# Kernel optimization log

Measured on AMD Instinct MI355X. Metric: run time of the kernel, lower is better.

Reference implementation:

```python
import jax, jax.numpy as jnp
import numpy as np

D_MODEL = 512
N_HEADS = 8
D_K = 64
D_V = 64
SEQ = 2048
BATCH = 4
WINDOW = 256  # mask_lenth
LN_EPS = 1e-5


def setup_inputs() -> dict:
    key = jax.random.key(0)
    ks = jax.random.split(key, 7)
    s = 1.0 / np.sqrt(D_MODEL)
    return {
        "input_Q": jax.random.normal(ks[0], (BATCH, SEQ, D_MODEL), jnp.float32),
        "input_K": jax.random.normal(ks[1], (BATCH, SEQ, D_MODEL), jnp.float32),
        "input_V": jax.random.normal(ks[2], (BATCH, SEQ, D_MODEL), jnp.float32),
        "W_Q": jax.random.normal(ks[3], (D_MODEL, N_HEADS * D_K), jnp.float32) * s,
        "W_K": jax.random.normal(ks[4], (D_MODEL, N_HEADS * D_K), jnp.float32) * s,
        "W_V": jax.random.normal(ks[5], (D_MODEL, N_HEADS * D_V), jnp.float32) * s,
        "W_fc": jax.random.normal(ks[6], (N_HEADS * D_V, D_MODEL), jnp.float32) * s,
    }


def _band_mask(n, w):
    # keep entries with i-(w-1) <= j <= i  (lower band of width w incl. diagonal)
    i = jnp.arange(n)[:, None]
    j = jnp.arange(n)[None, :]
    return (j <= i) & (j >= i - (w - 1))


def reference(input_Q, input_K, input_V, W_Q, W_K, W_V, W_fc):
    B, L, _ = input_Q.shape
    # projections -> [B, H, L, d]
    Q = (input_Q @ W_Q).reshape(B, L, N_HEADS, D_K).transpose(0, 2, 1, 3)
    K = (input_K @ W_K).reshape(B, L, N_HEADS, D_K).transpose(0, 2, 1, 3)
    V = (input_V @ W_V).reshape(B, L, N_HEADS, D_V).transpose(0, 2, 1, 3)

    scores = jnp.einsum("bhqd,bhkd->bhqk", Q, K) / np.sqrt(D_K)
    mask = _band_mask(L, WINDOW)  # [L, L] bool
    scores = jnp.where(mask[None, None], scores, -jnp.inf)
    attn = jax.nn.softmax(scores, axis=-1)
    context = jnp.einsum("bhqk,bhkd->bhqd", attn, V)  # [B,H,L,d_v]
    context = context.transpose(0, 2, 1, 3).reshape(B, L, N_HEADS * D_V)
    out = context @ W_fc + input_Q  # residual
    # LayerNorm (fresh nn.LayerNorm: gamma=1, beta=0)
    mu = jnp.mean(out, axis=-1, keepdims=True)
    var = jnp.var(out, axis=-1, keepdims=True)
    return (out - mu) * jax.lax.rsqrt(var + LN_EPS)
```

## Files before the change

kernel.cpp:

```cpp
#include <hip/hip_runtime.h>
#include <hip/hip_bf16.h>

#define D_MODEL 512
#define NH      8
#define SEQ     2048
#define BATCH   4
#define WINDOW  256
#define ROWS    (BATCH*SEQ)

typedef __attribute__((ext_vector_type(8))) short bf16x8;
typedef __attribute__((ext_vector_type(4))) float f32x4;
typedef __hip_bfloat16 bf16;

__device__ __forceinline__ f32x4 mfma16(bf16x8 a, bf16x8 b, f32x4 c) {
    return __builtin_amdgcn_mfma_f32_16x16x32_bf16(a, b, c, 0, 0, 0);
}

__device__ __forceinline__ void gload16(const void* g, void* l) {
    __builtin_amdgcn_global_load_lds((const __attribute__((address_space(1))) void*)g,
                                     (__attribute__((address_space(3))) void*)l, 16, 0, 0);
}

__device__ __forceinline__ unsigned f2bf_u(float f) {
    bf16 h = __float2bfloat16(f);
    return (unsigned)(*(unsigned short*)&h);
}

__global__ __launch_bounds__(256)
void wconv(const float* __restrict__ W0, const float* __restrict__ W1,
           const float* __restrict__ W2, const float* __restrict__ W3,
           bf16* __restrict__ Wt) {
    const int z = blockIdx.z;
    const float* W = (z == 0) ? W0 : (z == 1) ? W1 : (z == 2) ? W2 : W3;
    bf16* dst = Wt + (size_t)z * D_MODEL * D_MODEL;

    __shared__ float t[64][65];
    const int k0 = blockIdx.x * 64, n0 = blockIdx.y * 64;
    const int tid = threadIdx.x;

    #pragma unroll
    for (int i = 0; i < 16; ++i) {
        const int e = tid + 256 * i, r = e >> 6, c = e & 63;
        t[r][c] = W[(size_t)(k0 + r) * D_MODEL + n0 + c];
    }
    __syncthreads();
    #pragma unroll
    for (int i = 0; i < 16; ++i) {
        const int e = tid + 256 * i, r = e >> 6, c = e & 63;
        dst[(size_t)(n0 + r) * D_MODEL + k0 + c] = __float2bfloat16(t[c][r]);
    }
}

__global__ __launch_bounds__(256)
void proj_mfma(const float* __restrict__ Xq, const float* __restrict__ Xk,
               const float* __restrict__ Xv, const bf16* __restrict__ Wt,
               bf16* __restrict__ Qp, bf16* __restrict__ Kp, bf16* __restrict__ Vp) {
    const int z = blockIdx.z;
    const float* X = (z == 0) ? Xq : (z == 1) ? Xk : Xv;
    const bf16* W = Wt + (size_t)z * D_MODEL * D_MODEL;
    bf16* outp = (z == 0) ? Qp : (z == 1) ? Kp : Vp;

    __shared__ bf16 Asw[128 * 64];
    __shared__ bf16 Bsw[128 * 64];

    const int tid = threadIdx.x;
    const int lane = tid & 63, w = tid >> 6;
    const int wr = w >> 1, wc = w & 1;
    const int row0 = blockIdx.x * 128, col0 = blockIdx.y * 128;
    const int g = lane >> 4, m16 = lane & 15;

    f32x4 acc[4][4] = {};

    for (int step = 0; step < 8; ++step) {
        const int k0 = step * 64;
        __syncthreads();
        #pragma unroll
        for (int i = 0; i < 4; ++i) {
            const int chunk = i * 256 + w * 64 + lane;
            const int n = chunk >> 3, s = chunk & 7;
            gload16(W + (size_t)(col0 + n) * D_MODEL + k0 + ((s ^ (n & 7)) * 8),
                    &Bsw[(size_t)(i * 256 + w * 64) * 8]);
        }
        #pragma unroll
        for (int i = 0; i < 4; ++i) {
            const int chunk = i * 256 + tid;
            const int m = chunk >> 3, s = chunk & 7;
            const float* gp = X + (size_t)(row0 + m) * D_MODEL + k0 + ((s ^ (m & 7)) * 8);
            const float4 f0 = *(const float4*)gp;
            const float4 f1 = *(const float4*)(gp + 4);
            int4 pk;
            pk.x = f2bf_u(f0.x) | (f2bf_u(f0.y) << 16);
            pk.y = f2bf_u(f0.z) | (f2bf_u(f0.w) << 16);
            pk.z = f2bf_u(f1.x) | (f2bf_u(f1.y) << 16);
            pk.w = f2bf_u(f1.z) | (f2bf_u(f1.w) << 16);
            *(int4*)&Asw[m * 64 + s * 8] = pk;
        }
        __syncthreads();

        #pragma unroll
        for (int c = 0; c < 2; ++c) {
            bf16x8 af[4], bfr[4];
            #pragma unroll
            for (int mi = 0; mi < 4; ++mi) {
                const int m = wr * 64 + mi * 16 + m16;
                const int slot = (c * 4 + g) ^ (m & 7);
                af[mi] = *(const bf16x8*)&Asw[m * 64 + slot * 8];
            }
            #pragma unroll
            for (int ni = 0; ni < 4; ++ni) {
                const int n = wc * 64 + ni * 16 + m16;
                const int slot = (c * 4 + g) ^ (n & 7);
                bfr[ni] = *(const bf16x8*)&Bsw[n * 64 + slot * 8];
            }
            #pragma unroll
            for (int mi = 0; mi < 4; ++mi)
                #pragma unroll
                for (int ni = 0; ni < 4; ++ni)
                    acc[mi][ni] = mfma16(af[mi], bfr[ni], acc[mi][ni]);
        }
    }

    if (z < 2) {
        #pragma unroll
        for (int mi = 0; mi < 4; ++mi)
            #pragma unroll
            for (int ni = 0; ni < 4; ++ni) {
                const int c = col0 + wc * 64 + ni * 16 + m16;
                const int h = c >> 6, d = c & 63;
                #pragma unroll
                for (int reg = 0; reg < 4; ++reg) {
                    const int r = row0 + wr * 64 + mi * 16 + g * 4 + reg;
                    const int b = r >> 11, l = r & (SEQ - 1);
                    outp[(((size_t)b * NH + h) * SEQ + l) * 64 + d] =
                        __float2bfloat16(acc[mi][ni][reg]);
                }
            }
    } else {
        #pragma unroll
        for (int mi = 0; mi < 4; ++mi)
            #pragma unroll
            for (int ni = 0; ni < 4; ++ni) {
                const int c = col0 + wc * 64 + ni * 16 + m16;
                const int h = c >> 6, d = c & 63;
                const int r = row0 + wr * 64 + mi * 16 + g * 4;
                const int b = r >> 11, l = r & (SEQ - 1);
                uint2 pv;
                pv.x = f2bf_u(acc[mi][ni][0]) | (f2bf_u(acc[mi][ni][1]) << 16);
                pv.y = f2bf_u(acc[mi][ni][2]) | (f2bf_u(acc[mi][ni][3]) << 16);
                *(uint2*)&outp[(((size_t)b * NH + h) * 64 + d) * SEQ + l] = pv;
            }
    }
}

__global__ __launch_bounds__(256)
void attn_mfma(const bf16* __restrict__ Qp, const bf16* __restrict__ Kp,
               const bf16* __restrict__ Vp, bf16* __restrict__ ctx) {
    __shared__ bf16 Qs[64][72];
    __shared__ bf16 Ks[64][72];
    __shared__ bf16 Vt[64][72];
    __shared__ bf16 Ps[4][16][72];

    const int bh = blockIdx.y, b = bh >> 3, h = bh & 7;
    const int q0 = blockIdx.x * 64;
    const int tid = threadIdx.x;
    const int lane = tid & 63, w = tid >> 6;
    const int g = lane >> 4, m16 = lane & 15;

    const size_t kvbase = (size_t)bh * SEQ * 64;
    const size_t vtbase = (size_t)bh * 64 * SEQ;

    #pragma unroll
    for (int i = 0; i < 2; ++i) {
        const int chunk = i * 256 + tid, r = chunk >> 3, s = chunk & 7;
        *(int4*)&Qs[r][s * 8] = *(const int4*)(Qp + kvbase + (size_t)(q0 + r) * 64 + s * 8);
    }
    __syncthreads();

    bf16x8 qf[2];
    #pragma unroll
    for (int c = 0; c < 2; ++c)
        qf[c] = *(const bf16x8*)&Qs[w * 16 + m16][c * 32 + g * 8];

    f32x4 o[4] = {};
    float rs = 0.f;

    int klo = q0 - (WINDOW - 1); if (klo < 0) klo = 0;
    const int kt0 = klo >> 6, kt1 = q0 >> 6;
    const int qg = q0 + w * 16 + m16;

    for (int kt = kt0; kt <= kt1; ++kt) {
        const int k0 = kt * 64;
        __syncthreads();
        #pragma unroll
        for (int i = 0; i < 2; ++i) {
            const int chunk = i * 256 + tid, r = chunk >> 3, s = chunk & 7;
            *(int4*)&Ks[r][s * 8] = *(const int4*)(Kp + kvbase + (size_t)(k0 + r) * 64 + s * 8);
            *(int4*)&Vt[r][s * 8] = *(const int4*)(Vp + vtbase + (size_t)r * SEQ + k0 + s * 8);
        }
        __syncthreads();

        f32x4 st[4] = {};
        #pragma unroll
        for (int c = 0; c < 2; ++c) {
            bf16x8 kf[4];
            #pragma unroll
            for (int f = 0; f < 4; ++f)
                kf[f] = *(const bf16x8*)&Ks[f * 16 + m16][c * 32 + g * 8];
            #pragma unroll
            for (int f = 0; f < 4; ++f)
                st[f] = mfma16(kf[f], qf[c], st[f]);
        }

        const int masktype = (k0 == q0) ? 1 : ((k0 < q0 - 192) ? 2 : 0);
        #pragma unroll
        for (int f = 0; f < 4; ++f) {
            float p[4];
            #pragma unroll
            for (int reg = 0; reg < 4; ++reg) {
                const int kg = k0 + f * 16 + g * 4 + reg;
                bool valid = (masktype == 0) || (masktype == 1 ? (kg <= qg)
                                                              : (kg >= qg - (WINDOW - 1)));
                p[reg] = valid ? __expf(st[f][reg] * 0.125f) : 0.f;
                rs += p[reg];
            }
            uint2 pkv;
            pkv.x = f2bf_u(p[0]) | (f2bf_u(p[1]) << 16);
            pkv.y = f2bf_u(p[2]) | (f2bf_u(p[3]) << 16);
            *(uint2*)&Ps[w][m16][f * 16 + g * 4] = pkv;
        }

        #pragma unroll
        for (int c = 0; c < 2; ++c) {
            const bf16x8 pf = *(const bf16x8*)&Ps[w][m16][c * 32 + g * 8];
            #pragma unroll
            for (int f2 = 0; f2 < 4; ++f2) {
                const bf16x8 vf = *(const bf16x8*)&Vt[f2 * 16 + m16][c * 32 + g * 8];
                o[f2] = mfma16(pf, vf, o[f2]);
            }
        }
    }

    rs += __shfl_xor(rs, 16, 64);
    rs += __shfl_xor(rs, 32, 64);
    const float inv = 1.0f / rs;
    float invr[4];
    #pragma unroll
    for (int reg = 0; reg < 4; ++reg)
        invr[reg] = __shfl(inv, g * 4 + reg, 64);

    #pragma unroll
    for (int f2 = 0; f2 < 4; ++f2) {
        const int d = f2 * 16 + m16;
        #pragma unroll
        for (int reg = 0; reg < 4; ++reg) {
            const int qrow = w * 16 + g * 4 + reg;
            ctx[((size_t)b * SEQ + q0 + qrow) * D_MODEL + h * 64 + d] =
                __float2bfloat16(o[f2][reg] * invr[reg]);
        }
    }
}

__global__ __launch_bounds__(256)
void fc_mfma(const bf16* __restrict__ ctx, const bf16* __restrict__ Wt,
             const float* __restrict__ resid, float* __restrict__ out) {
    __shared__ bf16 Asw[128 * 64];
    __shared__ bf16 Bsw[128 * 64];

    const int tid = threadIdx.x;
    const int lane = tid & 63, w = tid >> 6;
    const int wr = w >> 1, wc = w & 1;
    const int row0 = blockIdx.x * 128, col0 = blockIdx.y * 128;
    const int g = lane >> 4, m16 = lane & 15;

    f32x4 acc[4][4] = {};

    for (int step = 0; step < 8; ++step) {
        const int k0 = step * 64;
        __syncthreads();
        #pragma unroll
        for (int i = 0; i < 4; ++i) {
            const int chunk = i * 256 + w * 64 + lane;
            const int m = chunk >> 3, s = chunk & 7;
            gload16(ctx + (size_t)(row0 + m) * D_MODEL + k0 + ((s ^ (m & 7)) * 8),
                    &Asw[(size_t)(i * 256 + w * 64) * 8]);
            gload16(Wt + (size_t)(col0 + m) * D_MODEL + k0 + ((s ^ (m & 7)) * 8),
                    &Bsw[(size_t)(i * 256 + w * 64) * 8]);
        }
        __syncthreads();

        #pragma unroll
        for (int c = 0; c < 2; ++c) {
            bf16x8 af[4], bfr[4];
            #pragma unroll
            for (int mi = 0; mi < 4; ++mi) {
                const int m = wr * 64 + mi * 16 + m16;
                const int slot = (c * 4 + g) ^ (m & 7);
                af[mi] = *(const bf16x8*)&Asw[m * 64 + slot * 8];
            }
            #pragma unroll
            for (int ni = 0; ni < 4; ++ni) {
                const int n = wc * 64 + ni * 16 + m16;
                const int slot = (c * 4 + g) ^ (n & 7);
                bfr[ni] = *(const bf16x8*)&Bsw[n * 64 + slot * 8];
            }
            #pragma unroll
            for (int mi = 0; mi < 4; ++mi)
                #pragma unroll
                for (int ni = 0; ni < 4; ++ni)
                    acc[mi][ni] = mfma16(af[mi], bfr[ni], acc[mi][ni]);
        }
    }

    #pragma unroll
    for (int mi = 0; mi < 4; ++mi)
        #pragma unroll
        for (int ni = 0; ni < 4; ++ni) {
            const int c = col0 + wc * 64 + ni * 16 + m16;
            #pragma unroll
            for (int reg = 0; reg < 4; ++reg) {
                const int r = row0 + wr * 64 + mi * 16 + g * 4 + reg;
                out[(size_t)r * D_MODEL + c] = acc[mi][ni][reg] + resid[(size_t)r * D_MODEL + c];
            }
        }
}

__global__ __launch_bounds__(256)
void ln_kernel(float* __restrict__ out) {
    const int row = blockIdx.x;
    float* p = out + (size_t)row * D_MODEL;
    const int tid = threadIdx.x;

    const float x0 = p[tid], x1 = p[tid + 256];
    float s  = x0 + x1;
    float s2 = x0 * x0 + x1 * x1;
    #pragma unroll
    for (int m = 1; m < 64; m <<= 1) {
        s  += __shfl_xor(s,  m, 64);
        s2 += __shfl_xor(s2, m, 64);
    }
    __shared__ float sa[4], sb[4];
    const int w = tid >> 6;
    if ((tid & 63) == 0) { sa[w] = s; sb[w] = s2; }
    __syncthreads();
    s  = sa[0] + sa[1] + sa[2] + sa[3];
    s2 = sb[0] + sb[1] + sb[2] + sb[3];

    const float mean = s * (1.0f / D_MODEL);
    const float var  = s2 * (1.0f / D_MODEL) - mean * mean;
    const float rstd = rsqrtf(var + 1e-5f);

    p[tid]       = (x0 - mean) * rstd;
    p[tid + 256] = (x1 - mean) * rstd;
}

extern "C" void kernel_launch(void* const* d_in, const int* in_sizes, int n_in,
                              void* d_out, int out_size, void* d_ws, size_t ws_size,
                              hipStream_t stream) {
    const float* inQ = (const float*)d_in[0];
    const float* inK = (const float*)d_in[1];
    const float* inV = (const float*)d_in[2];
    const float* WQ  = (const float*)d_in[3];
    const float* WK  = (const float*)d_in[4];
    const float* WV  = (const float*)d_in[5];
    const float* Wfc = (const float*)d_in[6];
    float* out = (float*)d_out;

    bf16* ws = (bf16*)d_ws;
    const size_t WSZ = (size_t)D_MODEL * D_MODEL;
    const size_t NE  = (size_t)BATCH * NH * SEQ * 64;
    bf16* Wt   = ws;
    bf16* Qp   = ws + 4 * WSZ;
    bf16* Kp   = Qp + NE;
    bf16* Vp   = Kp + NE;
    bf16* ctxb = Vp + NE;

    wconv<<<dim3(8, 8, 4), 256, 0, stream>>>(WQ, WK, WV, Wfc, Wt);
    proj_mfma<<<dim3(ROWS / 128, D_MODEL / 128, 3), 256, 0, stream>>>(
        inQ, inK, inV, Wt, Qp, Kp, Vp);
    attn_mfma<<<dim3(SEQ / 64, BATCH * NH), 256, 0, stream>>>(Qp, Kp, Vp, ctxb);
    fc_mfma<<<dim3(ROWS / 128, D_MODEL / 128), 256, 0, stream>>>(
        ctxb, Wt + 3 * WSZ, inQ, out);
    ln_kernel<<<ROWS, 256, 0, stream>>>(out);
}
```

Measured before the change: 170.7 us.

## Double-buffer LDS tiles in projection, attention and FC kernels to overlap loads

Adds ping-pong shared-memory buffers to the projection, attention and output-FC kernels. The next K-slice or KV tile is prefetched while MFMAs run on the current one, which removes one barrier per iteration. Attention now stages K/V/Q through direct global-to-LDS loads with an XOR swizzle instead of padded arrays. Float-to-bf16 packing uses a paired conversion intrinsic, and LayerNorm uses float2 accesses. The cost is doubled LDS use, which may lower occupancy, and more live registers for the prefetched fp32 A tile.

```diff
diff --git a/kernel.cpp b/kernel.cpp
--- a/kernel.cpp
+++ b/kernel.cpp
@@ -24,6 +24,12 @@
 __device__ __forceinline__ unsigned f2bf_u(float f) {
     bf16 h = __float2bfloat16(f);
     return (unsigned)(*(unsigned short*)&h);
+}
+
+__device__ __forceinline__ unsigned pack2(float lo, float hi) {
+    float2 t; t.x = lo; t.y = hi;
+    __hip_bfloat162 h = __float22bfloat162_rn(t);
+    return *(unsigned*)&h;
 }
 
 __global__ __launch_bounds__(256)
@@ -60,8 +66,8 @@
     const bf16* W = Wt + (size_t)z * D_MODEL * D_MODEL;
     bf16* outp = (z == 0) ? Qp : (z == 1) ? Kp : Vp;
 
-    __shared__ bf16 Asw[128 * 64];
-    __shared__ bf16 Bsw[128 * 64];
+    __shared__ bf16 Asw[2][128 * 64];
+    __shared__ bf16 Bsw[2][128 * 64];
 
     const int tid = threadIdx.x;
     const int lane = tid & 63, w = tid >> 6;
@@ -70,32 +76,50 @@
     const int g = lane >> 4, m16 = lane & 15;
 
     f32x4 acc[4][4] = {};
-
-    for (int step = 0; step < 8; ++step) {
-        const int k0 = step * 64;
-        __syncthreads();
+    float4 a0[4], a1[4];
+
+    auto stageB = [&](int buf, int k0) {
         #pragma unroll
         for (int i = 0; i < 4; ++i) {
             const int chunk = i * 256 + w * 64 + lane;
             const int n = chunk >> 3, s = chunk & 7;
             gload16(W + (size_t)(col0 + n) * D_MODEL + k0 + ((s ^ (n & 7)) * 8),
-                    &Bsw[(size_t)(i * 256 + w * 64) * 8]);
-        }
+                    &Bsw[buf][(i * 256 + w * 64) * 8]);
+        }
+    };
+    auto loadA = [&](int k0) {
         #pragma unroll
         for (int i = 0; i < 4; ++i) {
             const int chunk = i * 256 + tid;
             const int m = chunk >> 3, s = chunk & 7;
             const float* gp = X + (size_t)(row0 + m) * D_MODEL + k0 + ((s ^ (m & 7)) * 8);
-            const float4 f0 = *(const float4*)gp;
-            const float4 f1 = *(const float4*)(gp + 4);
+            a0[i] = *(const float4*)gp;
+            a1[i] = *(const float4*)(gp + 4);
+        }
+    };
+    auto writeA = [&](int buf) {
+        #pragma unroll
+        for (int i = 0; i < 4; ++i) {
+            const int chunk = i * 256 + tid;
+            const int m = chunk >> 3, s = chunk & 7;
             int4 pk;
-            pk.x = f2bf_u(f0.x) | (f2bf_u(f0.y) << 16);
-            pk.y = f2bf_u(f0.z) | (f2bf_u(f0.w) << 16);
-            pk.z = f2bf_u(f1.x) | (f2bf_u(f1.y) << 16);
-            pk.w = f2bf_u(f1.z) | (f2bf_u(f1.w) << 16);
-            *(int4*)&Asw[m * 64 + s * 8] = pk;
-        }
-        __syncthreads();
+            pk.x = pack2(a0[i].x, a0[i].y);
+            pk.y = pack2(a0[i].z, a0[i].w);
+            pk.z = pack2(a1[i].x, a1[i].y);
+            pk.w = pack2(a1[i].z, a1[i].w);
+            *(int4*)&Asw[buf][m * 64 + s * 8] = pk;
+        }
+    };
+
+    stageB(0, 0);
+    loadA(0);
+    writeA(0);
+    __syncthreads();
+
+    int cur = 0;
+    for (int step = 0; step < 8; ++step) {
+        const int k0n = (step + 1) * 64;
+        if (step < 7) { stageB(cur ^ 1, k0n); loadA(k0n); }
 
         #pragma unroll
         for (int c = 0; c < 2; ++c) {
@@ -104,13 +128,13 @@
             for (int mi = 0; mi < 4; ++mi) {
                 const int m = wr * 64 + mi * 16 + m16;
                 const int slot = (c * 4 + g) ^ (m & 7);
-                af[mi] = *(const bf16x8*)&Asw[m * 64 + slot * 8];
+                af[mi] = *(const bf16x8*)&Asw[cur][m * 64 + slot * 8];
             }
             #pragma unroll
             for (int ni = 0; ni < 4; ++ni) {
                 const int n = wc * 64 + ni * 16 + m16;
                 const int slot = (c * 4 + g) ^ (n & 7);
-                bfr[ni] = *(const bf16x8*)&Bsw[n * 64 + slot * 8];
+                bfr[ni] = *(const bf16x8*)&Bsw[cur][n * 64 + slot * 8];
             }
             #pragma unroll
             for (int mi = 0; mi < 4; ++mi)
@@ -118,6 +142,12 @@
                 for (int ni = 0; ni < 4; ++ni)
                     acc[mi][ni] = mfma16(af[mi], bfr[ni], acc[mi][ni]);
         }
+
+        if (step < 7) {
+            writeA(cur ^ 1);
+            __syncthreads();
+        }
+        cur ^= 1;
     }
 
     if (z < 2) {
@@ -155,10 +185,10 @@
 __global__ __launch_bounds__(256)
 void attn_mfma(const bf16* __restrict__ Qp, const bf16* __restrict__ Kp,
                const bf16* __restrict__ Vp, bf16* __restrict__ ctx) {
-    __shared__ bf16 Qs[64][72];
-    __shared__ bf16 Ks[64][72];
-    __shared__ bf16 Vt[64][72];
-    __shared__ bf16 Ps[4][16][72];
+    __shared__ bf16 Qs[64 * 64];
+    __shared__ bf16 Ks[2][64 * 64];
+    __shared__ bf16 Vt[2][64 * 64];
+    __shared__ bf16 Ps[4][16 * 64];
 
     const int bh = blockIdx.y, b = bh >> 3, h = bh & 7;
     const int q0 = blockIdx.x * 64;
@@ -169,43 +199,56 @@
     const size_t kvbase = (size_t)bh * SEQ * 64;
     const size_t vtbase = (size_t)bh * 64 * SEQ;
 
+    auto stageKV = [&](int buf, int k0) {
+        #pragma unroll
+        for (int i = 0; i < 2; ++i) {
+            const int chunk = i * 256 + tid;
+            const int r = chunk >> 3, s = chunk & 7;
+            gload16(Kp + kvbase + (size_t)(k0 + r) * 64 + ((s ^ (r & 7)) * 8),
+                    &Ks[buf][(i * 256 + w * 64) * 8]);
+            gload16(Vp + vtbase + (size_t)r * SEQ + k0 + ((s ^ (r & 7)) * 8),
+                    &Vt[buf][(i * 256 + w * 64) * 8]);
+        }
+    };
+
+    int klo = q0 - (WINDOW - 1); if (klo < 0) klo = 0;
+    const int kt0 = klo >> 6, kt1 = q0 >> 6;
+
     #pragma unroll
     for (int i = 0; i < 2; ++i) {
-        const int chunk = i * 256 + tid, r = chunk >> 3, s = chunk & 7;
-        *(int4*)&Qs[r][s * 8] = *(const int4*)(Qp + kvbase + (size_t)(q0 + r) * 64 + s * 8);
-    }
+        const int chunk = i * 256 + tid;
+        const int r = chunk >> 3, s = chunk & 7;
+        gload16(Qp + kvbase + (size_t)(q0 + r) * 64 + ((s ^ (r & 7)) * 8),
+                &Qs[(i * 256 + w * 64) * 8]);
+    }
+    stageKV(0, kt0 * 64);
     __syncthreads();
 
     bf16x8 qf[2];
     #pragma unroll
-    for (int c = 0; c < 2; ++c)
-        qf[c] = *(const bf16x8*)&Qs[w * 16 + m16][c * 32 + g * 8];
+    for (int c = 0; c < 2; ++c) {
+        const int r = w * 16 + m16;
+        qf[c] = *(const bf16x8*)&Qs[r * 64 + (((c * 4 + g) ^ (m16 & 7)) * 8)];
+    }
 
     f32x4 o[4] = {};
     float rs = 0.f;
-
-    int klo = q0 - (WINDOW - 1); if (klo < 0) klo = 0;
-    const int kt0 = klo >> 6, kt1 = q0 >> 6;
     const int qg = q0 + w * 16 + m16;
 
+    int cur = 0;
     for (int kt = kt0; kt <= kt1; ++kt) {
         const int k0 = kt * 64;
-        __syncthreads();
-        #pragma unroll
-        for (int i = 0; i < 2; ++i) {
-            const int chunk = i * 256 + tid, r = chunk >> 3, s = chunk & 7;
-            *(int4*)&Ks[r][s * 8] = *(const int4*)(Kp + kvbase + (size_t)(k0 + r) * 64 + s * 8);
-            *(int4*)&Vt[r][s * 8] = *(const int4*)(Vp + vtbase + (size_t)r * SEQ + k0 + s * 8);
-        }
-        __syncthreads();
+        if (kt < kt1) stageKV(cur ^ 1, (kt + 1) * 64);
 
         f32x4 st[4] = {};
         #pragma unroll
         for (int c = 0; c < 2; ++c) {
             bf16x8 kf[4];
             #pragma unroll
-            for (int f = 0; f < 4; ++f)
-                kf[f] = *(const bf16x8*)&Ks[f * 16 + m16][c * 32 + g * 8];
+            for (int f = 0; f < 4; ++f) {
+                const int r = f * 16 + m16;
+                kf[f] = *(const bf16x8*)&Ks[cur][r * 64 + (((c * 4 + g) ^ (m16 & 7)) * 8)];
+            }
             #pragma unroll
             for (int f = 0; f < 4; ++f)
                 st[f] = mfma16(kf[f], qf[c], st[f]);
@@ -224,20 +267,27 @@
                 rs += p[reg];
             }
             uint2 pkv;
-            pkv.x = f2bf_u(p[0]) | (f2bf_u(p[1]) << 16);
-            pkv.y = f2bf_u(p[2]) | (f2bf_u(p[3]) << 16);
-            *(uint2*)&Ps[w][m16][f * 16 + g * 4] = pkv;
+            pkv.x = pack2(p[0], p[1]);
+            pkv.y = pack2(p[2], p[3]);
+            const int slot = (f * 2 + (g >> 1)) ^ (m16 & 7);
+            *(uint2*)&Ps[w][m16 * 64 + slot * 8 + (g & 1) * 4] = pkv;
         }
 
         #pragma unroll
         for (int c = 0; c < 2; ++c) {
-            const bf16x8 pf = *(const bf16x8*)&Ps[w][m16][c * 32 + g * 8];
+            const bf16x8 pf =
+                *(const bf16x8*)&Ps[w][m16 * 64 + (((c * 4 + g) ^ (m16 & 7)) * 8)];
             #pragma unroll
             for (int f2 = 0; f2 < 4; ++f2) {
-                const bf16x8 vf = *(const bf16x8*)&Vt[f2 * 16 + m16][c * 32 + g * 8];
+                const int r = f2 * 16 + m16;
+                const bf16x8 vf =
+                    *(const bf16x8*)&Vt[cur][r * 64 + (((c * 4 + g) ^ (m16 & 7)) * 8)];
                 o[f2] = mfma16(pf, vf, o[f2]);
             }
         }
+
+        if (kt < kt1) __syncthreads();
+        cur ^= 1;
     }
 
     rs += __shfl_xor(rs, 16, 64);
@@ -263,8 +313,8 @@
 __global__ __launch_bounds__(256)
 void fc_mfma(const bf16* __restrict__ ctx, const bf16* __restrict__ Wt,
              const float* __restrict__ resid, float* __restrict__ out) {
-    __shared__ bf16 Asw[128 * 64];
-    __shared__ bf16 Bsw[128 * 64];
+    __shared__ bf16 Asw[2][128 * 64];
+    __shared__ bf16 Bsw[2][128 * 64];
 
     const int tid = threadIdx.x;
     const int lane = tid & 63, w = tid >> 6;
@@ -274,19 +324,24 @@
 
     f32x4 acc[4][4] = {};
 
-    for (int step = 0; step < 8; ++step) {
-        const int k0 = step * 64;
-        __syncthreads();
+    auto stage = [&](int buf, int k0) {
         #pragma unroll
         for (int i = 0; i < 4; ++i) {
             const int chunk = i * 256 + w * 64 + lane;
             const int m = chunk >> 3, s = chunk & 7;
             gload16(ctx + (size_t)(row0 + m) * D_MODEL + k0 + ((s ^ (m & 7)) * 8),
-                    &Asw[(size_t)(i * 256 + w * 64) * 8]);
+                    &Asw[buf][(i * 256 + w * 64) * 8]);
             gload16(Wt + (size_t)(col0 + m) * D_MODEL + k0 + ((s ^ (m & 7)) * 8),
-                    &Bsw[(size_t)(i * 256 + w * 64) * 8]);
-        }
-        __syncthreads();
+                    &Bsw[buf][(i * 256 + w * 64) * 8]);
+        }
+    };
+
+    stage(0, 0);
+    __syncthreads();
+
+    int cur = 0;
+    for (int step = 0; step < 8; ++step) {
+        if (step < 7) stage(cur ^ 1, (step + 1) * 64);
 
         #pragma unroll
         for (int c = 0; c < 2; ++c) {
@@ -295,13 +350,13 @@
             for (int mi = 0; mi < 4; ++mi) {
                 const int m = wr * 64 + mi * 16 + m16;
                 const int slot = (c * 4 + g) ^ (m & 7);
-                af[mi] = *(const bf16x8*)&Asw[m * 64 + slot * 8];
+                af[mi] = *(const bf16x8*)&Asw[cur][m * 64 + slot * 8];
             }
             #pragma unroll
             for (int ni = 0; ni < 4; ++ni) {
                 const int n = wc * 64 + ni * 16 + m16;
                 const int slot = (c * 4 + g) ^ (n & 7);
-                bfr[ni] = *(const bf16x8*)&Bsw[n * 64 + slot * 8];
+                bfr[ni] = *(const bf16x8*)&Bsw[cur][n * 64 + slot * 8];
             }
             #pragma unroll
             for (int mi = 0; mi < 4; ++mi)
@@ -309,6 +364,9 @@
                 for (int ni = 0; ni < 4; ++ni)
                     acc[mi][ni] = mfma16(af[mi], bfr[ni], acc[mi][ni]);
         }
+
+        if (step < 7) __syncthreads();
+        cur ^= 1;
     }
 
     #pragma unroll
@@ -330,9 +388,9 @@
     float* p = out + (size_t)row * D_MODEL;
     const int tid = threadIdx.x;
 
-    const float x0 = p[tid], x1 = p[tid + 256];
-    float s  = x0 + x1;
-    float s2 = x0 * x0 + x1 * x1;
+    float2 x = *(float2*)&p[tid * 2];
+    float s  = x.x + x.y;
+    float s2 = x.x * x.x + x.y * x.y;
     #pragma unroll
     for (int m = 1; m < 64; m <<= 1) {
         s  += __shfl_xor(s,  m, 64);
@@ -349,8 +407,9 @@
     const float var  = s2 * (1.0f / D_MODEL) - mean * mean;
     const float rstd = rsqrtf(var + 1e-5f);
 
-    p[tid]       = (x0 - mean) * rstd;
-    p[tid + 256] = (x1 - mean) * rstd;
+    x.x = (x.x - mean) * rstd;
+    x.y = (x.y - mean) * rstd;
+    *(float2*)&p[tid * 2] = x;
 }
 
 extern "C" void kernel_launch(void* const* d_in, const int* in_sizes, int n_in,
```

After: 177.7 us. 4.1% more time.
